# Kernel tuning notes

Hardware: AMD Instinct MI355X
Metric: run time of the kernel (lower is better)

## Reference

```python
import jax, jax.numpy as jnp
import numpy as np

D_MODEL, D_HEAD, N_HEADS, D_MLP = 1024, 64, 16, 4096


def setup_inputs() -> dict:
    key = jax.random.key(0)
    ks = jax.random.split(key, 12)
    # kaiming_normal_ on torch (fan_in = last dim for these layouts)
    def kn(k, shape, fan_in):
        return jax.random.normal(k, shape, dtype=jnp.float32) * jnp.sqrt(2.0 / fan_in)
    return {
        "x": jax.random.normal(ks[0], (4, 2048, D_MODEL), dtype=jnp.float32),
        "ln1_w": jnp.ones((D_MODEL,), jnp.float32),
        "ln1_b": jnp.zeros((D_MODEL,), jnp.float32),
        "W_Q": kn(ks[1], (N_HEADS, D_HEAD, D_MODEL), D_MODEL),
        "b_Q": jnp.zeros((N_HEADS, D_HEAD), jnp.float32),
        "W_K": kn(ks[2], (N_HEADS, D_HEAD, D_MODEL), D_MODEL),
        "b_K": jnp.zeros((N_HEADS, D_HEAD), jnp.float32),
        "W_V": kn(ks[3], (N_HEADS, D_HEAD, D_MODEL), D_MODEL),
        "b_V": jnp.zeros((N_HEADS, D_HEAD), jnp.float32),
        "W_O": kn(ks[4], (N_HEADS, D_MODEL, D_HEAD), D_HEAD),
        "b_O": jnp.zeros((D_MODEL,), jnp.float32),
        "ln2_w": jnp.ones((D_MODEL,), jnp.float32),
        "ln2_b": jnp.zeros((D_MODEL,), jnp.float32),
        "W_in": kn(ks[5], (D_MLP, D_MODEL), D_MODEL),
        "b_in": jnp.zeros((D_MLP,), jnp.float32),
        "W_out": kn(ks[6], (D_MODEL, D_MLP), D_MLP),
        "b_out": jnp.zeros((D_MODEL,), jnp.float32),
    }


def _layernorm(x, w, b, eps=1e-5):
    mu = jnp.mean(x, axis=-1, keepdims=True)
    var = jnp.var(x, axis=-1, keepdims=True)
    return (x - mu) * jax.lax.rsqrt(var + eps) * w + b


def reference(x, ln1_w, ln1_b, W_Q, b_Q, W_K, b_K, W_V, b_V, W_O, b_O,
              ln2_w, ln2_b, W_in, b_in, W_out, b_out):
    # --- pre-LN attention ---
    x_ln = _layernorm(x, ln1_w, ln1_b)
    Q = jnp.einsum('btd,nhd->btnh', x_ln, W_Q) + b_Q  # [B,S,H,Dh]
    K = jnp.einsum('btd,nhd->btnh', x_ln, W_K) + b_K
    V = jnp.einsum('btd,nhd->btnh', x_ln, W_V) + b_V
    scores = jnp.einsum('bqnh,bknh->bnqk', Q, K) / jnp.sqrt(
        jnp.asarray(Q.shape[-1], Q.dtype))  # [B,H,S,S]
    attn = jax.nn.softmax(scores, axis=-1)
    ctx = jnp.einsum('bnqk,bknh->bqnh', attn, V)  # [B,S,H,Dh]
    attn_out = jnp.einsum('btnh,ndh->btd', ctx, W_O) + b_O
    x_attn = attn_out + x
    # --- pre-LN MLP ---
    x_ln2 = _layernorm(x_attn, ln2_w, ln2_b)
    acts = jax.nn.gelu(jnp.einsum('btd,md->btm', x_ln2, W_in) + b_in,
                       approximate=False)
    mlp_out = jnp.einsum('btm,dm->btd', acts, W_out) + b_out
    return mlp_out + x_attn
```

## Files before the change

kernel.cpp:

```cpp
#include <hip/hip_runtime.h>
#include <hip/hip_bf16.h>
#include <stdint.h>

typedef __bf16 bf16;
typedef __attribute__((ext_vector_type(8))) __bf16 bf16x8;
typedef __attribute__((ext_vector_type(4))) __bf16 bf16x4;
typedef __attribute__((ext_vector_type(4))) float f32x4;

#define DEV __device__ __forceinline__

static constexpr int BB = 4, SS = 2048, DM = 1024, NH = 16, DH = 64, DMLP = 4096;
static constexpr int MR = BB * SS;

DEV void gload_lds16(const void* g, void* l) {
  __builtin_amdgcn_global_load_lds(
      (const __attribute__((address_space(1))) unsigned*)g,
      (__attribute__((address_space(3))) unsigned*)l, 16, 0, 0);
}

DEV uint32_t pk2(float a, float b) {
  bf16 x = (bf16)a, y = (bf16)b;
  uint16_t xa = __builtin_bit_cast(uint16_t, x), ya = __builtin_bit_cast(uint16_t, y);
  return (uint32_t)xa | ((uint32_t)ya << 16);
}

__global__ void k_prep_qkv(const float* __restrict__ wq, const float* __restrict__ wk,
                           const float* __restrict__ wv, const float* __restrict__ bq,
                           const float* __restrict__ bk, const float* __restrict__ bv,
                           bf16* __restrict__ wdst, float* __restrict__ bdst) {
  int i = blockIdx.x * 256 + threadIdx.x;
  int which = i >> 20, r = i & 1048575;
  const float* src = (which == 0) ? wq : (which == 1) ? wk : wv;
  wdst[i] = (bf16)src[r];
  if (i < 3072)
    bdst[i] = (i < 1024) ? bq[i] : (i < 2048) ? bk[i - 1024] : bv[i - 2048];
}

__global__ void k_prep_wo(const float* __restrict__ wo, bf16* __restrict__ dst) {
  int i = blockIdx.x * 256 + threadIdx.x;
  int d = i >> 10, k = i & 1023;
  int n = k >> 6, hh = k & 63;
  dst[i] = (bf16)wo[((size_t)n << 16) + (d << 6) + hh];
}

__global__ void k_convert(const float* __restrict__ s, bf16* __restrict__ d) {
  int i = blockIdx.x * 256 + threadIdx.x;
  float4 v = ((const float4*)s)[i];
  bf16x4 o; o[0]=(bf16)v.x; o[1]=(bf16)v.y; o[2]=(bf16)v.z; o[3]=(bf16)v.w;
  ((bf16x4*)d)[i] = o;
}

__global__ __launch_bounds__(256)
void k_ln(const float* __restrict__ xin, const float* __restrict__ w,
          const float* __restrict__ bvec, bf16* __restrict__ out) {
  const int row = blockIdx.x, tid = threadIdx.x;
  const float4 v = ((const float4*)(xin + (size_t)row * 1024))[tid];
  float s = v.x + v.y + v.z + v.w;
  float ss = v.x*v.x + v.y*v.y + v.z*v.z + v.w*v.w;
  #pragma unroll
  for (int m = 1; m < 64; m <<= 1) { s += __shfl_xor(s, m); ss += __shfl_xor(ss, m); }
  __shared__ float red[8];
  if ((tid & 63) == 0) { red[tid >> 6] = s; red[4 + (tid >> 6)] = ss; }
  __syncthreads();
  const float S  = red[0] + red[1] + red[2] + red[3];
  const float SQ = red[4] + red[5] + red[6] + red[7];
  const float mu = S * (1.f / 1024.f);
  const float rs = rsqrtf(fmaxf(SQ * (1.f / 1024.f) - mu * mu, 0.f) + 1e-5f);
  const float4 wv = ((const float4*)w)[tid];
  const float4 bv = ((const float4*)bvec)[tid];
  bf16x4 o;
  o[0] = (bf16)((v.x - mu) * rs * wv.x + bv.x);
  o[1] = (bf16)((v.y - mu) * rs * wv.y + bv.y);
  o[2] = (bf16)((v.z - mu) * rs * wv.z + bv.z);
  o[3] = (bf16)((v.w - mu) * rs * wv.w + bv.w);
  ((bf16x4*)(out + (size_t)row * 1024))[tid] = o;
}

enum { E_QKV = 0, E_OPROJ = 1, E_GELU = 2, E_FINAL = 3 };

template <int EPI>
__global__ __launch_bounds__(256, 2)
void k_gemm(const bf16* __restrict__ A, const bf16* __restrict__ Bw,
            const float* __restrict__ bias, const float* __restrict__ resid,
            void* __restrict__ Cout, int M, int N, int K) {
  __shared__ bf16 lA[128 * 32];
  __shared__ bf16 lB[128 * 32];
  const int nbn = N >> 7;
  const int nwg = gridDim.x;
  int wg = blockIdx.x;
  wg = (wg & 7) * (nwg >> 3) + (wg >> 3);
  const int bm = wg / nbn, bn = wg % nbn;
  const int tid = threadIdx.x, w = tid >> 6, l = tid & 63;
  const int wr = w >> 1, wc = w & 1;

  const int srow = w * 32 + (l >> 2);
  const int scb  = (l & 3) * 16;
  const char* gA = (const char*)(A + ((size_t)(bm * 128) + srow) * K) + scb;
  const char* gB = (const char*)(Bw + ((size_t)(bn * 128) + srow) * K) + scb;
  const size_t rstride = (size_t)K * 2 * 16;
  char* lAp = (char*)lA + w * 2048;
  char* lBp = (char*)lB + w * 2048;

  f32x4 acc[4][4] = {};

  const int nk = K >> 5;
  for (int kt = 0; kt < nk; ++kt) {
    __syncthreads();
    const size_t ko = (size_t)kt * 64;
    gload_lds16(gA + ko, lAp);
    gload_lds16(gA + ko + rstride, lAp + 1024);
    gload_lds16(gB + ko, lBp);
    gload_lds16(gB + ko + rstride, lBp + 1024);
    asm volatile("s_waitcnt vmcnt(0)" ::: "memory");
    __syncthreads();

    bf16x8 af[4], bfr[4];
    #pragma unroll
    for (int mi = 0; mi < 4; ++mi)
      af[mi] = *(const bf16x8*)&lA[(wr * 64 + mi * 16 + (l & 15)) * 32 + (l >> 4) * 8];
    #pragma unroll
    for (int ni = 0; ni < 4; ++ni)
      bfr[ni] = *(const bf16x8*)&lB[(wc * 64 + ni * 16 + (l & 15)) * 32 + (l >> 4) * 8];
    #pragma unroll
    for (int mi = 0; mi < 4; ++mi)
      #pragma unroll
      for (int ni = 0; ni < 4; ++ni)
        acc[mi][ni] = __builtin_amdgcn_mfma_f32_16x16x32_bf16(af[mi], bfr[ni], acc[mi][ni], 0, 0, 0);
  }

  const int row0 = bm * 128 + wr * 64 + ((l >> 4) << 2);
  const int col0 = bn * 128 + wc * 64 + (l & 15);
  #pragma unroll
  for (int mi = 0; mi < 4; ++mi) {
    #pragma unroll
    for (int ni = 0; ni < 4; ++ni) {
      const int col = col0 + ni * 16;
      const float bv = bias[col];
      #pragma unroll
      for (int r = 0; r < 4; ++r) {
        const int row = row0 + mi * 16 + r;
        float v = acc[mi][ni][r] + bv;
        if (EPI == E_GELU) v = 0.5f * v * (1.0f + erff(v * 0.70710678f));
        if (EPI == E_OPROJ || EPI == E_FINAL) v += resid[(size_t)row * N + col];
        if (EPI == E_OPROJ || EPI == E_FINAL) ((float*)Cout)[(size_t)row * N + col] = v;
        else                                  ((bf16*)Cout)[(size_t)row * N + col] = (bf16)v;
      }
    }
  }
}

__global__ __launch_bounds__(256)
void k_attn(const bf16* __restrict__ qkv, bf16* __restrict__ ctx) {
  __shared__ bf16 lQ[64 * 64], lK[64 * 64], lV[64 * 64];
  const int tid = threadIdx.x, w = tid >> 6, l = tid & 63;
  const int g = l >> 4, r15 = l & 15;
  const int qt = blockIdx.x, hd = blockIdx.y, b = blockIdx.z;

  const bf16* Qg = qkv + (size_t)(b * SS + qt * 64) * 3072 + hd * 64;
  const bf16* Kg = qkv + (size_t)(b * SS) * 3072 + 1024 + hd * 64;
  const bf16* Vg = Kg + 1024;

  {
    const int row = w * 16 + (l >> 3), cs = l & 7;
    char* lp = (char*)lQ + w * 2048;
    gload_lds16((const char*)(Qg + (size_t)row * 3072) + ((cs ^ (row & 7)) * 16), lp);
    const int row2 = row + 8;
    gload_lds16((const char*)(Qg + (size_t)row2 * 3072) + ((cs ^ (row2 & 7)) * 16), lp + 1024);
  }
  asm volatile("s_waitcnt vmcnt(0)" ::: "memory");
  __syncthreads();

  bf16x8 bq[2];
  {
    const int qrow = w * 16 + r15;
    #pragma unroll
    for (int c = 0; c < 2; ++c) {
      const int slot = (c * 4 + g) ^ (qrow & 7);
      bq[c] = *(const bf16x8*)((const char*)lQ + qrow * 128 + slot * 16);
    }
  }

  const int vk = (l >> 5) * 4 + ((l >> 1) & 3);
  const int vd = ((l >> 3) & 3) * 16 + (l & 1) * 8;

  const uint32_t vbase =
      (uint32_t)(uintptr_t)(__attribute__((address_space(3))) bf16*)lV + g * 1024 + r15 * 8;

  float m_run = -1e30f, l_run = 0.f;
  f32x4 oacc[4] = {};

  for (int kv = 0; kv < SS / 64; ++kv) {
    __syncthreads();
    {
      const int row = w * 16 + (l >> 3), cs = l & 7;
      char* lp = (char*)lK + w * 2048;
      const bf16* Kt = Kg + (size_t)(kv * 64) * 3072;
      gload_lds16((const char*)(Kt + (size_t)row * 3072) + ((cs ^ (row & 7)) * 16), lp);
      const int row2 = row + 8;
      gload_lds16((const char*)(Kt + (size_t)row2 * 3072) + ((cs ^ (row2 & 7)) * 16), lp + 1024);
    }
    {
      const bf16* Vt = Vg + (size_t)(kv * 64) * 3072;
      char* lp = (char*)lV + w * 1024;
      gload_lds16(Vt + (size_t)(w * 8 + vk) * 3072 + vd, lp);
      gload_lds16(Vt + (size_t)(w * 8 + vk + 32) * 3072 + vd, lp + 4096);
    }
    asm volatile("s_waitcnt vmcnt(0)" ::: "memory");
    __syncthreads();

    f32x4 s[4] = {};
    #pragma unroll
    for (int kt4 = 0; kt4 < 4; ++kt4) {
      const int krow = kt4 * 16 + r15;
      #pragma unroll
      for (int c = 0; c < 2; ++c) {
        const int slot = (c * 4 + g) ^ (krow & 7);
        bf16x8 kf = *(const bf16x8*)((const char*)lK + krow * 128 + slot * 16);
        s[kt4] = __builtin_amdgcn_mfma_f32_16x16x32_bf16(kf, bq[c], s[kt4], 0, 0, 0);
      }
    }
    #pragma unroll
    for (int kt4 = 0; kt4 < 4; ++kt4) s[kt4] *= 0.125f;

    float pmax = -1e30f;
    #pragma unroll
    for (int kt4 = 0; kt4 < 4; ++kt4)
      #pragma unroll
      for (int r = 0; r < 4; ++r) pmax = fmaxf(pmax, s[kt4][r]);
    pmax = fmaxf(pmax, __shfl_xor(pmax, 16));
    pmax = fmaxf(pmax, __shfl_xor(pmax, 32));
    const float mn = fmaxf(m_run, pmax);
    const float scl = __expf(m_run - mn);
    m_run = mn;
    float rsum = 0.f;
    #pragma unroll
    for (int kt4 = 0; kt4 < 4; ++kt4)
      #pragma unroll
      for (int r = 0; r < 4; ++r) {
        const float p = __expf(s[kt4][r] - m_run);
        s[kt4][r] = p;
        rsum += p;
      }
    rsum += __shfl_xor(rsum, 16);
    rsum += __shfl_xor(rsum, 32);
    l_run = l_run * scl + rsum;
    #pragma unroll
    for (int dt = 0; dt < 4; ++dt) oacc[dt] *= scl;

    uint32_t Dw[4][2];
    #pragma unroll
    for (int kt4 = 0; kt4 < 4; ++kt4) {
      Dw[kt4][0] = pk2(s[kt4][0], s[kt4][1]);
      Dw[kt4][1] = pk2(s[kt4][2], s[kt4][3]);
    }

    union PF { bf16x8 v; uint32_t u[4]; } pf[2];
    const int s0 = (((g & 1) * 2) * 16 + r15) * 4;
    const int s1 = s0 + 64;
    const bool hiKt = (g >> 1);
    #pragma unroll
    for (int hh = 0; hh < 2; ++hh) {
      #pragma unroll
      for (int w2 = 0; w2 < 2; ++w2) {
        const int a0 = __builtin_amdgcn_ds_bpermute(s0, (int)Dw[hh * 2][w2]);
        const int a1 = __builtin_amdgcn_ds_bpermute(s0, (int)Dw[hh * 2 + 1][w2]);
        const int b0 = __builtin_amdgcn_ds_bpermute(s1, (int)Dw[hh * 2][w2]);
        const int b1 = __builtin_amdgcn_ds_bpermute(s1, (int)Dw[hh * 2 + 1][w2]);
        pf[hh].u[w2]     = (uint32_t)(hiKt ? a1 : a0);
        pf[hh].u[2 + w2] = (uint32_t)(hiKt ? b1 : b0);
      }
    }

    bf16x4 tr[4][2][2];
    #pragma unroll
    for (int dt = 0; dt < 4; ++dt)
      #pragma unroll
      for (int hh = 0; hh < 2; ++hh)
        #pragma unroll
        for (int sub = 0; sub < 2; ++sub) {
          const uint32_t a = vbase + hh * 4096 + sub * 512 + dt * 128;
          asm volatile("ds_read_b64_tr_b16 %0, %1" : "=v"(tr[dt][hh][sub]) : "v"(a));
        }
    asm volatile("s_waitcnt lgkmcnt(0)" ::: "memory");
    __builtin_amdgcn_sched_barrier(0);

    #pragma unroll
    for (int dt = 0; dt < 4; ++dt) {
      #pragma unroll
      for (int hh = 0; hh < 2; ++hh) {
        bf16x8 av;
        #pragma unroll
        for (int j = 0; j < 4; ++j) { av[j] = tr[dt][hh][0][j]; av[4 + j] = tr[dt][hh][1][j]; }
        oacc[dt] = __builtin_amdgcn_mfma_f32_16x16x32_bf16(av, pf[hh].v, oacc[dt], 0, 0, 0);
      }
    }
  }

  const float inv = 1.0f / l_run;
  const size_t row_out = (size_t)(b * SS + qt * 64 + w * 16 + r15);
  #pragma unroll
  for (int dt = 0; dt < 4; ++dt) {
    bf16x4 o4;
    #pragma unroll
    for (int r = 0; r < 4; ++r) o4[r] = (bf16)(oacc[dt][r] * inv);
    *(bf16x4*)(ctx + row_out * 1024 + hd * 64 + dt * 16 + g * 4) = o4;
  }
}

extern "C" void kernel_launch(void* const* d_in, const int* in_sizes, int n_in,
                              void* d_out, int out_size, void* d_ws, size_t ws_size,
                              hipStream_t stream) {
  const float* x    = (const float*)d_in[0];
  const float* ln1w = (const float*)d_in[1];
  const float* ln1b = (const float*)d_in[2];
  const float* WQ   = (const float*)d_in[3];
  const float* bQ   = (const float*)d_in[4];
  const float* WK   = (const float*)d_in[5];
  const float* bK   = (const float*)d_in[6];
  const float* WV   = (const float*)d_in[7];
  const float* bV   = (const float*)d_in[8];
  const float* WO   = (const float*)d_in[9];
  const float* bO   = (const float*)d_in[10];
  const float* ln2w = (const float*)d_in[11];
  const float* ln2b = (const float*)d_in[12];
  const float* Win  = (const float*)d_in[13];
  const float* bin  = (const float*)d_in[14];
  const float* Wout = (const float*)d_in[15];
  const float* bout = (const float*)d_in[16];

  char* ws = (char*)d_ws;
  const size_t NEED = (size_t)3072*1024*2 + (size_t)1024*1024*2 + (size_t)4096*1024*2
                    + (size_t)1024*4096*2 + 3072*4 + (size_t)MR*1024*4
                    + (size_t)MR*1024*2 + (size_t)MR*3072*2 + (size_t)MR*1024*2;
  if (ws_size < NEED) return;

  bf16*  wqkv = (bf16*)ws;  ws += (size_t)3072 * 1024 * 2;
  bf16*  wo   = (bf16*)ws;  ws += (size_t)1024 * 1024 * 2;
  bf16*  win  = (bf16*)ws;  ws += (size_t)4096 * 1024 * 2;
  bf16*  wout = (bf16*)ws;  ws += (size_t)1024 * 4096 * 2;
  float* bqkv = (float*)ws; ws += 3072 * 4;
  float* xattn= (float*)ws; ws += (size_t)MR * 1024 * 4;
  bf16*  xln  = (bf16*)ws;  ws += (size_t)MR * 1024 * 2;
  bf16*  qkv  = (bf16*)ws;  ws += (size_t)MR * 3072 * 2;
  bf16*  ctx  = (bf16*)ws;  ws += (size_t)MR * 1024 * 2;
  bf16*  acts = qkv;

  k_prep_qkv<<<3 * 1048576 / 256, 256, 0, stream>>>(WQ, WK, WV, bQ, bK, bV, wqkv, bqkv);
  k_prep_wo<<<1048576 / 256, 256, 0, stream>>>(WO, wo);
  k_convert<<<4194304 / 1024, 256, 0, stream>>>(Win, win);
  k_convert<<<4194304 / 1024, 256, 0, stream>>>(Wout, wout);

  k_ln<<<MR, 256, 0, stream>>>(x, ln1w, ln1b, xln);
  k_gemm<E_QKV><<<(MR / 128) * (3072 / 128), 256, 0, stream>>>(xln, wqkv, bqkv, nullptr, qkv, MR, 3072, 1024);
  k_attn<<<dim3(SS / 64, NH, BB), 256, 0, stream>>>(qkv, ctx);
  k_gemm<E_OPROJ><<<(MR / 128) * (1024 / 128), 256, 0, stream>>>(ctx, wo, bO, x, xattn, MR, 1024, 1024);
  k_ln<<<MR, 256, 0, stream>>>(xattn, ln2w, ln2b, xln);
  k_gemm<E_GELU><<<(MR / 128) * (4096 / 128), 256, 0, stream>>>(xln, win, bin, nullptr, acts, MR, 4096, 1024);
  k_gemm<E_FINAL><<<(MR / 128) * (1024 / 128), 256, 0, stream>>>(acts, wout, bout, xattn, (float*)d_out, MR, 1024, 4096);
}
```

Before: 628.7 us.

## Replace GEMM with 256x256 tile, double-buffered, swizzled-LDS pipelined kernel

Replaces the 128x128, single-buffered GEMM with a 512-thread 256x256 tile kernel. It uses 64-wide K steps, double-buffered LDS (128KB) with XOR-swizzled layout, and interleaves async global->LDS loads with MFMA phases using barriers and s_setprio. The goal is to hide global load latency, cut LDS bank conflicts, and raise arithmetic intensity per tile. In exchange it uses much more LDS, which limits occupancy to one block per CU. The small grids for O-proj and final GEMMs (128 blocks) may underfill the 256 CUs.

Result: slower. 647.2 us (+3.0%).

```diff
diff --git a/kernel.cpp b/kernel.cpp
--- a/kernel.cpp
+++ b/kernel.cpp
@@ -79,67 +79,126 @@
 enum { E_QKV = 0, E_OPROJ = 1, E_GELU = 2, E_FINAL = 3 };
 
 template <int EPI>
-__global__ __launch_bounds__(256, 2)
-void k_gemm(const bf16* __restrict__ A, const bf16* __restrict__ Bw,
-            const float* __restrict__ bias, const float* __restrict__ resid,
-            void* __restrict__ Cout, int M, int N, int K) {
-  __shared__ bf16 lA[128 * 32];
-  __shared__ bf16 lB[128 * 32];
-  const int nbn = N >> 7;
+__global__ __launch_bounds__(512, 2)
+void k_gemm256(const bf16* __restrict__ A, const bf16* __restrict__ Bw,
+               const float* __restrict__ bias, const float* __restrict__ resid,
+               void* __restrict__ Cout, int M, int N, int K) {
+  __shared__ char lds[131072];
+  const int nbn = N >> 8;
   const int nwg = gridDim.x;
   int wg = blockIdx.x;
   wg = (wg & 7) * (nwg >> 3) + (wg >> 3);
   const int bm = wg / nbn, bn = wg % nbn;
   const int tid = threadIdx.x, w = tid >> 6, l = tid & 63;
-  const int wr = w >> 1, wc = w & 1;
-
-  const int srow = w * 32 + (l >> 2);
-  const int scb  = (l & 3) * 16;
-  const char* gA = (const char*)(A + ((size_t)(bm * 128) + srow) * K) + scb;
-  const char* gB = (const char*)(Bw + ((size_t)(bn * 128) + srow) * K) + scb;
-  const size_t rstride = (size_t)K * 2 * 16;
-  char* lAp = (char*)lA + w * 2048;
-  char* lBp = (char*)lB + w * 2048;
-
-  f32x4 acc[4][4] = {};
-
-  const int nk = K >> 5;
-  for (int kt = 0; kt < nk; ++kt) {
-    __syncthreads();
-    const size_t ko = (size_t)kt * 64;
-    gload_lds16(gA + ko, lAp);
-    gload_lds16(gA + ko + rstride, lAp + 1024);
-    gload_lds16(gB + ko, lBp);
-    gload_lds16(gB + ko + rstride, lBp + 1024);
-    asm volatile("s_waitcnt vmcnt(0)" ::: "memory");
-    __syncthreads();
-
-    bf16x8 af[4], bfr[4];
-    #pragma unroll
-    for (int mi = 0; mi < 4; ++mi)
-      af[mi] = *(const bf16x8*)&lA[(wr * 64 + mi * 16 + (l & 15)) * 32 + (l >> 4) * 8];
-    #pragma unroll
-    for (int ni = 0; ni < 4; ++ni)
-      bfr[ni] = *(const bf16x8*)&lB[(wc * 64 + ni * 16 + (l & 15)) * 32 + (l >> 4) * 8];
-    #pragma unroll
-    for (int mi = 0; mi < 4; ++mi)
+  const int wr = w >> 2, wc = w & 3;
+  const int g = l >> 4, r15 = l & 15;
+
+  const int sL = tid >> 3;
+  const int sp = (tid & 7) ^ (sL & 7);
+  const int srow = sL * 2 + (sp >> 2);
+  const size_t Kb = (size_t)K * 2;
+  const char* gA0 = (const char*)A + ((size_t)(bm * 256) + srow) * Kb + (sp & 3) * 16;
+  const char* gB0 = (const char*)Bw + ((size_t)(bn * 256) + srow) * Kb + (sp & 3) * 16;
+  const int sdst = w * 1024 + l * 16;
+
+  const int fslot = (((r15 & 1) << 2) | g) ^ (r15 >> 1);
+  const int ard = wr * 8192 + (r15 >> 1) * 128 + fslot * 16;
+  const int brd = 32768 + wc * 4096 + (r15 >> 1) * 128 + fslot * 16;
+
+  f32x4 acc[8][4] = {};
+  const int nk = K >> 6;
+
+#define STG(bufb, mat, kk, T) do {                                             \
+    const char* gsrc = ((mat) ? gB0 : gA0) + (size_t)(T) * 128 + (kk) * 64;    \
+    char* ldst = lds + (bufb) * 65536 + (mat) * 32768 + (kk) * 16384 + sdst;   \
+    gload_lds16(gsrc, ldst);                                                   \
+    gload_lds16(gsrc + 128 * Kb, ldst + 8192);                                 \
+  } while (0)
+
+  STG(0, 0, 0, 0); STG(0, 1, 0, 0); STG(0, 0, 1, 0); STG(0, 1, 1, 0);
+  if (nk > 1) { STG(1, 0, 0, 1); STG(1, 1, 0, 1); }
+  asm volatile("s_waitcnt vmcnt(4)" ::: "memory");
+  __builtin_amdgcn_s_barrier();
+  __builtin_amdgcn_sched_barrier(0);
+
+  for (int T = 0; T < nk; ++T) {
+    const int cur = T & 1, nxt = cur ^ 1;
+    const char* lbuf = lds + cur * 65536;
+    bf16x8 afr[4], bfr[4];
+
+    #pragma unroll
+    for (int i = 0; i < 4; ++i) afr[i] = *(const bf16x8*)(lbuf + ard + i * 1024);
+    #pragma unroll
+    for (int i = 0; i < 4; ++i) bfr[i] = *(const bf16x8*)(lbuf + brd + i * 1024);
+    if (T + 1 < nk) STG(nxt, 0, 1, T + 1);
+    __builtin_amdgcn_s_barrier(); __builtin_amdgcn_sched_barrier(0);
+    __builtin_amdgcn_s_setprio(1);
+    #pragma unroll
+    for (int fi = 0; fi < 4; ++fi)
       #pragma unroll
       for (int ni = 0; ni < 4; ++ni)
-        acc[mi][ni] = __builtin_amdgcn_mfma_f32_16x16x32_bf16(af[mi], bfr[ni], acc[mi][ni], 0, 0, 0);
-  }
-
-  const int row0 = bm * 128 + wr * 64 + ((l >> 4) << 2);
-  const int col0 = bn * 128 + wc * 64 + (l & 15);
+        acc[fi][ni] = __builtin_amdgcn_mfma_f32_16x16x32_bf16(afr[fi], bfr[ni], acc[fi][ni], 0, 0, 0);
+    __builtin_amdgcn_s_setprio(0);
+    __builtin_amdgcn_s_barrier(); __builtin_amdgcn_sched_barrier(0);
+
+    #pragma unroll
+    for (int i = 0; i < 4; ++i) afr[i] = *(const bf16x8*)(lbuf + ard + (4 + i) * 1024);
+    if (T + 1 < nk) STG(nxt, 1, 1, T + 1);
+    __builtin_amdgcn_s_barrier(); __builtin_amdgcn_sched_barrier(0);
+    __builtin_amdgcn_s_setprio(1);
+    #pragma unroll
+    for (int fi = 0; fi < 4; ++fi)
+      #pragma unroll
+      for (int ni = 0; ni < 4; ++ni)
+        acc[4 + fi][ni] = __builtin_amdgcn_mfma_f32_16x16x32_bf16(afr[fi], bfr[ni], acc[4 + fi][ni], 0, 0, 0);
+    __builtin_amdgcn_s_setprio(0);
+    asm volatile("s_waitcnt vmcnt(4)" ::: "memory");
+    __builtin_amdgcn_s_barrier(); __builtin_amdgcn_sched_barrier(0);
+
+    #pragma unroll
+    for (int i = 0; i < 4; ++i) afr[i] = *(const bf16x8*)(lbuf + 16384 + ard + i * 1024);
+    #pragma unroll
+    for (int i = 0; i < 4; ++i) bfr[i] = *(const bf16x8*)(lbuf + 16384 + brd + i * 1024);
+    if (T + 2 < nk) STG(cur, 0, 0, T + 2);
+    __builtin_amdgcn_s_barrier(); __builtin_amdgcn_sched_barrier(0);
+    __builtin_amdgcn_s_setprio(1);
+    #pragma unroll
+    for (int fi = 0; fi < 4; ++fi)
+      #pragma unroll
+      for (int ni = 0; ni < 4; ++ni)
+        acc[fi][ni] = __builtin_amdgcn_mfma_f32_16x16x32_bf16(afr[fi], bfr[ni], acc[fi][ni], 0, 0, 0);
+    __builtin_amdgcn_s_setprio(0);
+    __builtin_amdgcn_s_barrier(); __builtin_amdgcn_sched_barrier(0);
+
+    #pragma unroll
+    for (int i = 0; i < 4; ++i) afr[i] = *(const bf16x8*)(lbuf + 16384 + ard + (4 + i) * 1024);
+    if (T + 2 < nk) STG(cur, 1, 0, T + 2);
+    __builtin_amdgcn_s_barrier(); __builtin_amdgcn_sched_barrier(0);
+    __builtin_amdgcn_s_setprio(1);
+    #pragma unroll
+    for (int fi = 0; fi < 4; ++fi)
+      #pragma unroll
+      for (int ni = 0; ni < 4; ++ni)
+        acc[4 + fi][ni] = __builtin_amdgcn_mfma_f32_16x16x32_bf16(afr[fi], bfr[ni], acc[4 + fi][ni], 0, 0, 0);
+    __builtin_amdgcn_s_setprio(0);
+    if (T + 2 < nk) { asm volatile("s_waitcnt vmcnt(4)" ::: "memory"); }
+    else            { asm volatile("s_waitcnt vmcnt(0)" ::: "memory"); }
+    __builtin_amdgcn_s_barrier(); __builtin_amdgcn_sched_barrier(0);
+  }
+#undef STG
+
+  const int row0 = bm * 256 + wr * 128 + g * 4;
+  const int col0 = bn * 256 + wc * 64 + r15;
   #pragma unroll
-  for (int mi = 0; mi < 4; ++mi) {
-    #pragma unroll
-    for (int ni = 0; ni < 4; ++ni) {
-      const int col = col0 + ni * 16;
+  for (int fr = 0; fr < 8; ++fr) {
+    #pragma unroll
+    for (int fn = 0; fn < 4; ++fn) {
+      const int col = col0 + fn * 16;
       const float bv = bias[col];
       #pragma unroll
       for (int r = 0; r < 4; ++r) {
-        const int row = row0 + mi * 16 + r;
-        float v = acc[mi][ni][r] + bv;
+        const int row = row0 + fr * 16 + r;
+        float v = acc[fr][fn][r] + bv;
         if (EPI == E_GELU) v = 0.5f * v * (1.0f + erff(v * 0.70710678f));
         if (EPI == E_OPROJ || EPI == E_FINAL) v += resid[(size_t)row * N + col];
         if (EPI == E_OPROJ || EPI == E_FINAL) ((float*)Cout)[(size_t)row * N + col] = v;
@@ -351,10 +410,10 @@
   k_convert<<<4194304 / 1024, 256, 0, stream>>>(Wout, wout);
 
   k_ln<<<MR, 256, 0, stream>>>(x, ln1w, ln1b, xln);
-  k_gemm<E_QKV><<<(MR / 128) * (3072 / 128), 256, 0, stream>>>(xln, wqkv, bqkv, nullptr, qkv, MR, 3072, 1024);
+  k_gemm256<E_QKV><<<(MR / 256) * (3072 / 256), 512, 0, stream>>>(xln, wqkv, bqkv, nullptr, qkv, MR, 3072, 1024);
   k_attn<<<dim3(SS / 64, NH, BB), 256, 0, stream>>>(qkv, ctx);
-  k_gemm<E_OPROJ><<<(MR / 128) * (1024 / 128), 256, 0, stream>>>(ctx, wo, bO, x, xattn, MR, 1024, 1024);
+  k_gemm256<E_OPROJ><<<(MR / 256) * (1024 / 256), 512, 0, stream>>>(ctx, wo, bO, x, xattn, MR, 1024, 1024);
   k_ln<<<MR, 256, 0, stream>>>(xattn, ln2w, ln2b, xln);
-  k_gemm<E_GELU><<<(MR / 128) * (4096 / 128), 256, 0, stream>>>(xln, win, bin, nullptr, acts, MR, 4096, 1024);
-  k_gemm<E_FINAL><<<(MR / 128) * (1024 / 128), 256, 0, stream>>>(acts, wout, bout, xattn, (float*)d_out, MR, 1024, 4096);
-}
+  k_gemm256<E_GELU><<<(MR / 256) * (4096 / 256), 512, 0, stream>>>(xln, win, bin, nullptr, acts, MR, 4096, 1024);
+  k_gemm256<E_FINAL><<<(MR / 256) * (1024 / 256), 512, 0, stream>>>(acts, wout, bout, xattn, (float*)d_out, MR, 1024, 4096);
+}
```
